# Performance work log

Hardware: AMD Instinct MI355X
Metric: run time of the kernel (lower is better)

The kernel has to match this reference:

```python
import jax, jax.numpy as jnp
import numpy as np

NZ, N_GEN = 128, 10
H1, H2, IMG = 512, 1024, 784
BATCH = 4096


def setup_inputs() -> dict:
    key = jax.random.key(0)
    ks = jax.random.split(key, 5)
    z = jax.random.normal(ks[0], (BATCH, NZ), dtype=jnp.float32)
    g_idx = jax.random.randint(ks[1], (BATCH,), 0, N_GEN)
    # stacked per-generator MLP weights (fan-in scaled init)
    W1 = jax.random.normal(ks[2], (N_GEN, NZ, H1), dtype=jnp.float32) / np.sqrt(NZ)
    b1 = jnp.zeros((N_GEN, H1), dtype=jnp.float32)
    W2 = jax.random.normal(ks[3], (N_GEN, H1, H2), dtype=jnp.float32) / np.sqrt(H1)
    b2 = jnp.zeros((N_GEN, H2), dtype=jnp.float32)
    W3 = jax.random.normal(ks[4], (N_GEN, H2, IMG), dtype=jnp.float32) / np.sqrt(H2)
    b3 = jnp.zeros((N_GEN, IMG), dtype=jnp.float32)
    return {"z": z, "g_idx": g_idx, "W1": W1, "b1": b1, "W2": W2, "b2": b2, "W3": W3, "b3": b3}


def reference(z, g_idx, W1, b1, W2, b2, W3, b3):
    # Run ALL n_gen sub-generators for every sample (as the torch module does),
    # then gather the chosen branch per sample.
    h = jax.nn.relu(jnp.einsum('bz,gzh->bgh', z, W1) + b1)          # [B, G, H1]
    h = jax.nn.relu(jnp.einsum('bgh,ghk->bgk', h, W2) + b2)         # [B, G, H2]
    images = jnp.tanh(jnp.einsum('bgk,gki->bgi', h, W3) + b3)       # [B, G, IMG]
    # images[arange(B), g_idx]
    out = jnp.take_along_axis(images, g_idx[:, None, None], axis=1)[:, 0]  # [B, IMG]
    return out
```

## Files before the change

### kernel.cpp

```cpp
#include <hip/hip_runtime.h>
#include <math.h>

#define NZ    128
#define H1    512
#define H2    1024
#define IMG   784
#define IMGP  896
#define BATCH 4096
#define NGEN  10
#define MPAD  128

typedef _Float16 f16;
typedef __attribute__((ext_vector_type(8))) _Float16 half8;
typedef __attribute__((ext_vector_type(4))) float floatx4;

#define TB1 ((NZ / 64) * (H1 / 64) * NGEN)
#define TB2 ((H1 / 64) * (H2 / 64) * NGEN)
#define TB3 ((H2 / 64) * (IMGP / 64) * NGEN)

__device__ __forceinline__ void cp16(void* l, const void* g) {
    __builtin_amdgcn_global_load_lds((const __attribute__((address_space(1))) void*)g,
                                     (__attribute__((address_space(3))) void*)l, 16, 0, 0);
}

template<int K, int N, int NPAD>
__device__ __forceinline__ void t_tile(int idx, const float* __restrict__ W,
                                       f16* __restrict__ Wt, f16 (*L)[72]) {
    constexpr int KT = K / 64, NT = NPAD / 64;
    const int g  = idx / (KT * NT);
    const int r2 = idx % (KT * NT);
    const int k0 = (r2 % KT) * 64;
    const int n0 = (r2 / KT) * 64;
    const int t = threadIdx.x;
    {
        const int kk0 = t >> 4;
        const int nq  = (t & 15) * 4;
        #pragma unroll
        for (int it = 0; it < 4; ++it) {
            const int kk = kk0 + it * 16;
            float4 v = make_float4(0.f, 0.f, 0.f, 0.f);
            if (n0 + nq < N)
                v = *(const float4*)(W + ((size_t)g * K + (k0 + kk)) * N + n0 + nq);
            L[nq + 0][kk] = (f16)v.x;
            L[nq + 1][kk] = (f16)v.y;
            L[nq + 2][kk] = (f16)v.z;
            L[nq + 3][kk] = (f16)v.w;
        }
    }
    __syncthreads();
    {
        const int nn0 = t >> 3;
        const int kq  = (t & 7) * 8;
        #pragma unroll
        for (int it = 0; it < 2; ++it) {
            const int nn = nn0 + it * 32;
            *(half8*)(Wt + ((size_t)g * NPAD + (n0 + nn)) * K + k0 + kq) =
                *(const half8*)&L[nn][kq];
        }
    }
}

__global__ __launch_bounds__(256)
void prep(const float* __restrict__ W1, const float* __restrict__ W2,
          const float* __restrict__ W3, f16* __restrict__ W1t,
          f16* __restrict__ W2t, f16* __restrict__ W3t,
          const int* __restrict__ g_idx, int* __restrict__ seg,
          int* __restrict__ perm) {
    __shared__ f16 L[64][72];
    __shared__ int lc[NGEN];
    __shared__ int lb[NGEN + 1];
    int bid = blockIdx.x;
    if (bid == 0) {
        const int t = threadIdx.x;
        if (t < NGEN) lc[t] = 0;
        __syncthreads();
        int gv[BATCH / 256];
        #pragma unroll
        for (int i = 0; i < BATCH / 256; ++i) {
            gv[i] = g_idx[t + i * 256];
            atomicAdd(&lc[gv[i]], 1);
        }
        __syncthreads();
        if (t == 0) {
            int s = 0;
            for (int g = 0; g < NGEN; ++g) { lb[g] = s; s += lc[g]; }
            lb[NGEN] = s;
        }
        __syncthreads();
        if (t <= NGEN) seg[t] = lb[t];
        if (t < NGEN) lc[t] = lb[t];
        __syncthreads();
        #pragma unroll
        for (int i = 0; i < BATCH / 256; ++i) {
            int p = atomicAdd(&lc[gv[i]], 1);
            perm[p] = t + i * 256;
        }
        return;
    }
    --bid;
    if (bid < TB1) { t_tile<NZ, H1, H1>(bid, W1, W1t, L); return; }
    bid -= TB1;
    if (bid < TB2) { t_tile<H1, H2, H2>(bid, W2, W2t, L); return; }
    bid -= TB2;
    t_tile<H2, IMG, IMGP>(bid, W3, W3t, L);
}

template<int K, int NOUT, int NPADB, int NM, int NN, int ACT, int SCATTER>
__global__ __launch_bounds__(256)
void gemm128(const f16* __restrict__ Ap, const f16* __restrict__ Wt,
             const float* __restrict__ bias, f16* __restrict__ Ch,
             float* __restrict__ Cout, const int* __restrict__ seg,
             const int* __restrict__ perm) {
    constexpr int NT  = K / 64;
    constexpr int NWG = NM * NN * NGEN;
    static_assert(NWG % 8 == 0, "gen-chunk swizzle needs NWG % 8 == 0");
    static_assert(NT >= 2, "pipeline assumes K >= 128");
    constexpr int CHUNK = NWG / 8;

    const int H = blockIdx.x;
    const int L = (H & 7) * CHUNK + (H >> 3);
    const int g   = L / (NM * NN);
    const int rem = L - g * (NM * NN);
    const int nt  = rem / NM;
    const int mt0 = rem - nt * NM;
    const int s0 = seg[g];
    const int ng = seg[g + 1] - s0;
    const int m0 = mt0 * 128;
    if (m0 >= ng) return;
    const int n0 = nt * 128;

    __shared__ f16 As[2 * 128 * 64];
    __shared__ f16 Bs[2 * 128 * 64];

    const int tid = threadIdx.x, lane = tid & 63, w = tid >> 6;

    const f16* ga[4]; const f16* gb[4]; int lo[4];
    #pragma unroll
    for (int j = 0; j < 4; ++j) {
        const int r   = w * 32 + j * 8 + (lane >> 3);
        const int swz = ((lane & 7) ^ ((r >> 1) & 7)) * 8;
        ga[j] = Ap + (size_t)(s0 + m0 + r) * K + swz;
        gb[j] = Wt + ((size_t)g * NPADB + n0 + r) * K + swz;
        lo[j] = (w * 32 + j * 8) * 64;
    }

    const int wm = (w & 1) * 64, wn = (w >> 1) * 64;
    const int lm = lane & 15, lq = lane >> 4;

    const int c = n0 + wn + 2 * lm;
    const bool in0 = (!SCATTER) || (c < NOUT);
    const bool in1 = (!SCATTER) || (c + 32 < NOUT);
    const float* bg = bias + (size_t)g * NOUT;
    const float bv0 = in0 ? bg[c]      : 0.f;
    const float bv1 = in0 ? bg[c + 1]  : 0.f;
    const float bv2 = in1 ? bg[c + 32] : 0.f;
    const float bv3 = in1 ? bg[c + 33] : 0.f;

    floatx4 acc[4][4] = {};

    auto stage = [&](int t, int b) {
        #pragma unroll
        for (int j = 0; j < 4; ++j) cp16(&As[b * 8192 + lo[j]], ga[j] + (size_t)t * 64);
        #pragma unroll
        for (int j = 0; j < 4; ++j) cp16(&Bs[b * 8192 + lo[j]], gb[j] + (size_t)t * 64);
    };
    stage(0, 0);
    __builtin_amdgcn_sched_barrier(0);
    stage(1, 1);

    for (int kc = 0; kc < NT; ++kc) {
        if (kc + 1 < NT) asm volatile("s_waitcnt vmcnt(8)" ::: "memory");
        else             asm volatile("s_waitcnt vmcnt(0)" ::: "memory");
        __builtin_amdgcn_sched_barrier(0);
        __builtin_amdgcn_s_barrier();
        __builtin_amdgcn_sched_barrier(0);

        const int cb = (kc & 1) * 8192;
        half8 a[2][4], b[2][4];
        #pragma unroll
        for (int ks = 0; ks < 2; ++ks) {
            #pragma unroll
            for (int mt = 0; mt < 4; ++mt) {
                const int r  = wm + mt * 16 + lm;
                const int pq = (ks * 4 + lq) ^ ((r >> 1) & 7);
                a[ks][mt] = *(const half8*)&As[cb + r * 64 + pq * 8];
            }
            #pragma unroll
            for (int nf = 0; nf < 4; ++nf) {
                const int r  = wn + (nf >> 1) * 32 + 2 * lm + (nf & 1);
                const int pq = (ks * 4 + lq) ^ ((r >> 1) & 7);
                b[ks][nf] = *(const half8*)&Bs[cb + r * 64 + pq * 8];
            }
        }
        asm volatile("s_waitcnt lgkmcnt(0)" ::: "memory");
        __builtin_amdgcn_sched_barrier(0);
        if (kc + 2 < NT) {
            __builtin_amdgcn_s_barrier();
            __builtin_amdgcn_sched_barrier(0);
            stage(kc + 2, kc & 1);
        }
        #pragma unroll
        for (int ks = 0; ks < 2; ++ks)
            #pragma unroll
            for (int mt = 0; mt < 4; ++mt)
                #pragma unroll
                for (int nf = 0; nf < 4; ++nf)
                    acc[mt][nf] = __builtin_amdgcn_mfma_f32_16x16x32_f16(
                        a[ks][mt], b[ks][nf], acc[mt][nf], 0, 0, 0);
    }

    #pragma unroll
    for (int mt = 0; mt < 4; ++mt)
        #pragma unroll
        for (int rr = 0; rr < 4; ++rr) {
            const int gr = m0 + wm + mt * 16 + lq * 4 + rr;
            if (gr >= ng) continue;
            float x0 = acc[mt][0][rr] + bv0;
            float x1 = acc[mt][1][rr] + bv1;
            float x2 = acc[mt][2][rr] + bv2;
            float x3 = acc[mt][3][rr] + bv3;
            if (ACT == 0) {
                x0 = fmaxf(x0, 0.f); x1 = fmaxf(x1, 0.f);
                x2 = fmaxf(x2, 0.f); x3 = fmaxf(x3, 0.f);
            } else {
                const float e0 = __expf(2.f * x0);
                const float e1 = __expf(2.f * x1);
                const float e2 = __expf(2.f * x2);
                const float e3 = __expf(2.f * x3);
                x0 = 1.f - 2.f / (e0 + 1.f);
                x1 = 1.f - 2.f / (e1 + 1.f);
                x2 = 1.f - 2.f / (e2 + 1.f);
                x3 = 1.f - 2.f / (e3 + 1.f);
            }
            if (SCATTER) {
                const size_t orow = (size_t)perm[s0 + gr];
                if (in0) *(float2*)&Cout[orow * NOUT + c]      = make_float2(x0, x1);
                if (in1) *(float2*)&Cout[orow * NOUT + c + 32] = make_float2(x2, x3);
            } else {
                union { uint u; f16 h[2]; } o0, o1;
                o0.h[0] = (f16)x0; o0.h[1] = (f16)x1;
                o1.h[0] = (f16)x2; o1.h[1] = (f16)x3;
                *(uint*)&Ch[(size_t)(s0 + gr) * NOUT + c]      = o0.u;
                *(uint*)&Ch[(size_t)(s0 + gr) * NOUT + c + 32] = o1.u;
            }
        }
}

__global__ __launch_bounds__(256)
void gemm_l1(const float* __restrict__ Az, const f16* __restrict__ Wt,
             const float* __restrict__ bias, f16* __restrict__ Ch,
             const int* __restrict__ seg, const int* __restrict__ perm) {
    constexpr int K = NZ, NOUT = H1, NPADB = H1, NM = 8, NN = 4;
    constexpr int NWG = NM * NN * NGEN, CHUNK = NWG / 8;
    const int H = blockIdx.x;
    const int L = (H & 7) * CHUNK + (H >> 3);
    const int g   = L / (NM * NN);
    const int rem = L - g * (NM * NN);
    const int nt  = rem / NM;
    const int mt0 = rem - nt * NM;
    const int s0 = seg[g];
    const int ng = seg[g + 1] - s0;
    const int m0 = mt0 * 128;
    if (m0 >= ng) return;
    const int n0 = nt * 128;

    __shared__ f16 As[2 * 8192];
    __shared__ f16 Bs[2 * 8192];
    const int tid = threadIdx.x, lane = tid & 63, w = tid >> 6;

    #pragma unroll
    for (int j = 0; j < 4; ++j) {
        const int r   = w * 32 + j * 8 + (lane >> 3);
        const int swz = ((lane & 7) ^ ((r >> 1) & 7)) * 8;
        const f16* gbj = Wt + ((size_t)g * NPADB + n0 + r) * K + swz;
        const int  loj = (w * 32 + j * 8) * 64;
        cp16(&Bs[loj],        gbj);
        cp16(&Bs[8192 + loj], gbj + 64);
    }
    int prow[4];
    #pragma unroll
    for (int p = 0; p < 4; ++p) {
        const int r = w * 32 + p * 8 + (lane >> 3);
        prow[p] = perm[min(s0 + m0 + r, BATCH - 1)];
    }
    #pragma unroll
    for (int t = 0; t < 2; ++t)
        #pragma unroll
        for (int p = 0; p < 4; ++p) {
            const int r = w * 32 + p * 8 + (lane >> 3);
            const float* src = Az + (size_t)prow[p] * K + t * 64 + (lane & 7) * 8;
            const float4 v0 = *(const float4*)src;
            const float4 v1 = *(const float4*)(src + 4);
            half8 h;
            h[0] = (f16)v0.x; h[1] = (f16)v0.y; h[2] = (f16)v0.z; h[3] = (f16)v0.w;
            h[4] = (f16)v1.x; h[5] = (f16)v1.y; h[6] = (f16)v1.z; h[7] = (f16)v1.w;
            const int pq = (lane & 7) ^ ((r >> 1) & 7);
            *(half8*)&As[t * 8192 + r * 64 + pq * 8] = h;
        }

    const int wm = (w & 1) * 64, wn = (w >> 1) * 64;
    const int lm = lane & 15, lq = lane >> 4;
    const int c = n0 + wn + 2 * lm;
    const float* bg = bias + (size_t)g * NOUT;
    const float bv0 = bg[c], bv1 = bg[c + 1], bv2 = bg[c + 32], bv3 = bg[c + 33];

    __syncthreads();

    floatx4 acc[4][4] = {};
    #pragma unroll
    for (int kc = 0; kc < 2; ++kc) {
        const int cb = kc * 8192;
        half8 a[2][4], b[2][4];
        #pragma unroll
        for (int ks = 0; ks < 2; ++ks) {
            #pragma unroll
            for (int mt = 0; mt < 4; ++mt) {
                const int r  = wm + mt * 16 + lm;
                const int pq = (ks * 4 + lq) ^ ((r >> 1) & 7);
                a[ks][mt] = *(const half8*)&As[cb + r * 64 + pq * 8];
            }
            #pragma unroll
            for (int nf = 0; nf < 4; ++nf) {
                const int r  = wn + (nf >> 1) * 32 + 2 * lm + (nf & 1);
                const int pq = (ks * 4 + lq) ^ ((r >> 1) & 7);
                b[ks][nf] = *(const half8*)&Bs[cb + r * 64 + pq * 8];
            }
        }
        #pragma unroll
        for (int ks = 0; ks < 2; ++ks)
            #pragma unroll
            for (int mt = 0; mt < 4; ++mt)
                #pragma unroll
                for (int nf = 0; nf < 4; ++nf)
                    acc[mt][nf] = __builtin_amdgcn_mfma_f32_16x16x32_f16(
                        a[ks][mt], b[ks][nf], acc[mt][nf], 0, 0, 0);
    }

    #pragma unroll
    for (int mt = 0; mt < 4; ++mt)
        #pragma unroll
        for (int rr = 0; rr < 4; ++rr) {
            const int gr = m0 + wm + mt * 16 + lq * 4 + rr;
            if (gr >= ng) continue;
            float x0 = fmaxf(acc[mt][0][rr] + bv0, 0.f);
            float x1 = fmaxf(acc[mt][1][rr] + bv1, 0.f);
            float x2 = fmaxf(acc[mt][2][rr] + bv2, 0.f);
            float x3 = fmaxf(acc[mt][3][rr] + bv3, 0.f);
            union { uint u; f16 h[2]; } o0, o1;
            o0.h[0] = (f16)x0; o0.h[1] = (f16)x1;
            o1.h[0] = (f16)x2; o1.h[1] = (f16)x3;
            *(uint*)&Ch[(size_t)(s0 + gr) * NOUT + c]      = o0.u;
            *(uint*)&Ch[(size_t)(s0 + gr) * NOUT + c + 32] = o1.u;
        }
}

extern "C" void kernel_launch(void* const* d_in, const int* in_sizes, int n_in,
                              void* d_out, int out_size, void* d_ws, size_t ws_size,
                              hipStream_t stream) {
    const float* z    = (const float*)d_in[0];
    const int*   gidx = (const int*)  d_in[1];
    const float* W1   = (const float*)d_in[2];
    const float* b1   = (const float*)d_in[3];
    const float* W2   = (const float*)d_in[4];
    const float* b2   = (const float*)d_in[5];
    const float* W3   = (const float*)d_in[6];
    const float* b3   = (const float*)d_in[7];
    float* out = (float*)d_out;

    char* ws = (char*)d_ws;
    size_t off = 0;
    auto alloc = [&](size_t bytes) { size_t o = off; off = (off + bytes + 255) & ~255ULL; return o; };
    int* seg  = (int*)(ws + alloc((size_t)(NGEN + 1) * 4));
    int* perm = (int*)(ws + alloc((size_t)(BATCH + MPAD) * 4));
    f16* h1p = (f16*)(ws + alloc((size_t)(BATCH + MPAD) * H1 * 2));
    f16* h2p = (f16*)(ws + alloc((size_t)(BATCH + MPAD) * H2 * 2));
    f16* W1t = (f16*)(ws + alloc((size_t)NGEN * H1 * NZ * 2));
    f16* W2t = (f16*)(ws + alloc((size_t)NGEN * H2 * H1 * 2));
    f16* W3t = (f16*)(ws + alloc((size_t)NGEN * IMGP * H2 * 2));

    prep<<<dim3(1 + TB1 + TB2 + TB3), dim3(256), 0, stream>>>(
        W1, W2, W3, W1t, W2t, W3t, gidx, seg, perm);

    gemm_l1<<<dim3(8 * 4 * NGEN), dim3(256), 0, stream>>>(
        z, W1t, b1, h1p, seg, perm);
    gemm128<H1, H2, H2, 8, 8, 0, 0><<<dim3(8 * 8 * NGEN), dim3(256), 0, stream>>>(
        h1p, W2t, b2, h2p, nullptr, seg, perm);
    gemm128<H2, IMG, IMGP, 8, 7, 1, 1><<<dim3(8 * 7 * NGEN), dim3(256), 0, stream>>>(
        h2p, W3t, b3, nullptr, out, seg, perm);
}
```

Measured before the change: 155.4 us.

## Fuse prep and three GEMM layers into one persistent kernel with grid barriers

Replaces the four separate launches with a single persistent kernel of 512 workgroups that moves through phases separated by atomic grid barriers. Each weight transpose is overlapped with the previous layer's GEMM. GEMM tiles are enumerated only for live row blocks per generator, so no workgroups launch just to exit. This removes launch gaps and idle tail time but adds barrier spin cost and a memset. It also relies on all 512 workgroups being co-resident (two per CU) to avoid deadlock.

```diff
diff --git a/kernel.cpp b/kernel.cpp
--- a/kernel.cpp
+++ b/kernel.cpp
@@ -9,6 +9,7 @@
 #define BATCH 4096
 #define NGEN  10
 #define MPAD  128
+#define NWORK 512
 
 typedef _Float16 f16;
 typedef __attribute__((ext_vector_type(8))) _Float16 half8;
@@ -23,9 +24,25 @@
                                      (__attribute__((address_space(3))) void*)l, 16, 0, 0);
 }
 
+__device__ __forceinline__ void gridbar(int* bar, int phase) {
+    __syncthreads();
+    if (threadIdx.x == 0) {
+        __threadfence();
+        __hip_atomic_fetch_add(&bar[phase], 1, __ATOMIC_RELEASE,
+                               __HIP_MEMORY_SCOPE_AGENT);
+        while (__hip_atomic_load(&bar[phase], __ATOMIC_ACQUIRE,
+                                 __HIP_MEMORY_SCOPE_AGENT) < NWORK)
+            __builtin_amdgcn_s_sleep(8);
+        __threadfence();
+    }
+    __syncthreads();
+}
+
 template<int K, int N, int NPAD>
-__device__ __forceinline__ void t_tile(int idx, const float* __restrict__ W,
-                                       f16* __restrict__ Wt, f16 (*L)[72]) {
+__device__ void t_item(int idx, const float* __restrict__ W,
+                       f16* __restrict__ Wt, char* smraw) {
+    f16 (*L)[72] = (f16(*)[72])smraw;
+    __syncthreads();
     constexpr int KT = K / 64, NT = NPAD / 64;
     const int g  = idx / (KT * NT);
     const int r2 = idx % (KT * NT);
@@ -60,79 +77,78 @@
     }
 }
 
-__global__ __launch_bounds__(256)
-void prep(const float* __restrict__ W1, const float* __restrict__ W2,
-          const float* __restrict__ W3, f16* __restrict__ W1t,
-          f16* __restrict__ W2t, f16* __restrict__ W3t,
-          const int* __restrict__ g_idx, int* __restrict__ seg,
-          int* __restrict__ perm) {
-    __shared__ f16 L[64][72];
-    __shared__ int lc[NGEN];
-    __shared__ int lb[NGEN + 1];
-    int bid = blockIdx.x;
-    if (bid == 0) {
-        const int t = threadIdx.x;
-        if (t < NGEN) lc[t] = 0;
-        __syncthreads();
-        int gv[BATCH / 256];
-        #pragma unroll
-        for (int i = 0; i < BATCH / 256; ++i) {
-            gv[i] = g_idx[t + i * 256];
-            atomicAdd(&lc[gv[i]], 1);
-        }
-        __syncthreads();
-        if (t == 0) {
-            int s = 0;
-            for (int g = 0; g < NGEN; ++g) { lb[g] = s; s += lc[g]; }
-            lb[NGEN] = s;
-        }
-        __syncthreads();
-        if (t <= NGEN) seg[t] = lb[t];
-        if (t < NGEN) lc[t] = lb[t];
-        __syncthreads();
-        #pragma unroll
-        for (int i = 0; i < BATCH / 256; ++i) {
-            int p = atomicAdd(&lc[gv[i]], 1);
-            perm[p] = t + i * 256;
-        }
-        return;
-    }
-    --bid;
-    if (bid < TB1) { t_tile<NZ, H1, H1>(bid, W1, W1t, L); return; }
-    bid -= TB1;
-    if (bid < TB2) { t_tile<H1, H2, H2>(bid, W2, W2t, L); return; }
-    bid -= TB2;
-    t_tile<H2, IMG, IMGP>(bid, W3, W3t, L);
-}
-
-template<int K, int NOUT, int NPADB, int NM, int NN, int ACT, int SCATTER>
-__global__ __launch_bounds__(256)
-void gemm128(const f16* __restrict__ Ap, const f16* __restrict__ Wt,
-             const float* __restrict__ bias, f16* __restrict__ Ch,
-             float* __restrict__ Cout, const int* __restrict__ seg,
-             const int* __restrict__ perm) {
-    constexpr int NT  = K / 64;
-    constexpr int NWG = NM * NN * NGEN;
-    static_assert(NWG % 8 == 0, "gen-chunk swizzle needs NWG % 8 == 0");
-    static_assert(NT >= 2, "pipeline assumes K >= 128");
-    constexpr int CHUNK = NWG / 8;
-
-    const int H = blockIdx.x;
-    const int L = (H & 7) * CHUNK + (H >> 3);
-    const int g   = L / (NM * NN);
-    const int rem = L - g * (NM * NN);
-    const int nt  = rem / NM;
-    const int mt0 = rem - nt * NM;
-    const int s0 = seg[g];
-    const int ng = seg[g + 1] - s0;
-    const int m0 = mt0 * 128;
-    if (m0 >= ng) return;
-    const int n0 = nt * 128;
-
-    __shared__ f16 As[2 * 128 * 64];
-    __shared__ f16 Bs[2 * 128 * 64];
-
+__device__ void hist_item(const int* __restrict__ g_idx, int* __restrict__ seg,
+                          int* __restrict__ perm, char* smraw) {
+    int* lc = (int*)smraw;
+    int* lb = lc + NGEN;
+    const int t = threadIdx.x;
+    __syncthreads();
+    if (t < NGEN) lc[t] = 0;
+    __syncthreads();
+    int gv[BATCH / 256];
+    #pragma unroll
+    for (int i = 0; i < BATCH / 256; ++i) {
+        gv[i] = g_idx[t + i * 256];
+        atomicAdd(&lc[gv[i]], 1);
+    }
+    __syncthreads();
+    if (t == 0) {
+        int s = 0;
+        #pragma unroll
+        for (int g = 0; g < NGEN; ++g) { lb[g] = s; s += lc[g]; }
+        lb[NGEN] = s;
+    }
+    __syncthreads();
+    if (t <= NGEN) seg[t] = lb[t];
+    if (t < NGEN) lc[t] = lb[t];
+    __syncthreads();
+    #pragma unroll
+    for (int i = 0; i < BATCH / 256; ++i) {
+        int p = atomicAdd(&lc[gv[i]], 1);
+        perm[p] = t + i * 256;
+    }
+}
+
+template<int NN>
+__device__ __forceinline__ int live_total(const int* __restrict__ seg) {
+    int s = 0;
+    #pragma unroll
+    for (int g = 0; g < NGEN; ++g)
+        s += (((seg[g + 1] - seg[g]) + 127) >> 7) * NN;
+    return s;
+}
+template<int NN>
+__device__ __forceinline__ void item_to_tile(const int* __restrict__ seg, int i,
+                                             int& g, int& s0, int& ng,
+                                             int& m0, int& n0) {
+    int base = 0;
+    #pragma unroll
+    for (int gg = 0; gg < NGEN; ++gg) {
+        const int s = seg[gg], e = seg[gg + 1];
+        const int cm = ((e - s) + 127) >> 7;
+        const int c  = cm * NN;
+        if (i >= base && i < base + c) {
+            const int loc = i - base;
+            g = gg; s0 = s; ng = e - s;
+            m0 = (loc % cm) * 128;
+            n0 = (loc / cm) * 128;
+        }
+        base += c;
+    }
+}
+
+template<int K, int NOUT, int NPADB, int ACT, int SCATTER>
+__device__ void gemm_item(int g, int s0, int ng, int m0, int n0,
+                          const f16* __restrict__ Ap, const f16* __restrict__ Wt,
+                          const float* __restrict__ bias, f16* __restrict__ Ch,
+                          float* __restrict__ Cout, const int* __restrict__ perm,
+                          char* smraw) {
+    constexpr int NT = K / 64;
+    f16* As = (f16*)smraw;
+    f16* Bs = (f16*)(smraw + 32768);
     const int tid = threadIdx.x, lane = tid & 63, w = tid >> 6;
+
+    __syncthreads();
 
     const f16* ga[4]; const f16* gb[4]; int lo[4];
     #pragma unroll
@@ -143,7 +159,6 @@
         gb[j] = Wt + ((size_t)g * NPADB + n0 + r) * K + swz;
         lo[j] = (w * 32 + j * 8) * 64;
     }
-
     const int wm = (w & 1) * 64, wn = (w >> 1) * 64;
     const int lm = lane & 15, lq = lane >> 4;
 
@@ -246,27 +261,16 @@
         }
 }
 
-__global__ __launch_bounds__(256)
-void gemm_l1(const float* __restrict__ Az, const f16* __restrict__ Wt,
-             const float* __restrict__ bias, f16* __restrict__ Ch,
-             const int* __restrict__ seg, const int* __restrict__ perm) {
-    constexpr int K = NZ, NOUT = H1, NPADB = H1, NM = 8, NN = 4;
-    constexpr int NWG = NM * NN * NGEN, CHUNK = NWG / 8;
-    const int H = blockIdx.x;
-    const int L = (H & 7) * CHUNK + (H >> 3);
-    const int g   = L / (NM * NN);
-    const int rem = L - g * (NM * NN);
-    const int nt  = rem / NM;
-    const int mt0 = rem - nt * NM;
-    const int s0 = seg[g];
-    const int ng = seg[g + 1] - s0;
-    const int m0 = mt0 * 128;
-    if (m0 >= ng) return;
-    const int n0 = nt * 128;
-
-    __shared__ f16 As[2 * 8192];
-    __shared__ f16 Bs[2 * 8192];
+__device__ void l1_item(int g, int s0, int ng, int m0, int n0,
+                        const float* __restrict__ Az, const f16* __restrict__ Wt,
+                        const float* __restrict__ bias, f16* __restrict__ Ch,
+                        const int* __restrict__ perm, char* smraw) {
+    constexpr int K = NZ, NOUT = H1, NPADB = H1;
+    f16* As = (f16*)smraw;
+    f16* Bs = (f16*)(smraw + 32768);
     const int tid = threadIdx.x, lane = tid & 63, w = tid >> 6;
+
+    __syncthreads();
 
     #pragma unroll
     for (int j = 0; j < 4; ++j) {
@@ -354,6 +358,58 @@
         }
 }
 
+__global__ __launch_bounds__(256, 2)
+void fused(const float* __restrict__ z, const int* __restrict__ gidx,
+           const float* __restrict__ W1, const float* __restrict__ b1,
+           const float* __restrict__ W2, const float* __restrict__ b2,
+           const float* __restrict__ W3, const float* __restrict__ b3,
+           float* __restrict__ out, int* seg, int* perm,
+           f16* h1p, f16* h2p, f16* W1t, f16* W2t, f16* W3t, int* bar) {
+    __shared__ __align__(16) char sm[65536];
+    const int bid = blockIdx.x;
+
+    for (int i = bid; i < 1 + TB1; i += NWORK) {
+        if (i == 0) hist_item(gidx, seg, perm, sm);
+        else        t_item<NZ, H1, H1>(i - 1, W1, W1t, sm);
+    }
+    gridbar(bar, 0);
+
+    {
+        const int nl = live_total<H1 / 128>(seg);
+        for (int i = bid; i < nl + TB2; i += NWORK) {
+            if (i < nl) {
+                int g, s0, ng, m0, n0;
+                item_to_tile<H1 / 128>(seg, i, g, s0, ng, m0, n0);
+                l1_item(g, s0, ng, m0, n0, z, W1t, b1, h1p, perm, sm);
+            } else t_item<H1, H2, H2>(i - nl, W2, W2t, sm);
+        }
+    }
+    gridbar(bar, 1);
+
+    {
+        const int nl = live_total<H2 / 128>(seg);
+        for (int i = bid; i < nl + TB3; i += NWORK) {
+            if (i < nl) {
+                int g, s0, ng, m0, n0;
+                item_to_tile<H2 / 128>(seg, i, g, s0, ng, m0, n0);
+                gemm_item<H1, H2, H2, 0, 0>(g, s0, ng, m0, n0, h1p, W2t, b2,
+                                            h2p, nullptr, perm, sm);
+            } else t_item<H2, IMG, IMGP>(i - nl, W3, W3t, sm);
+        }
+    }
+    gridbar(bar, 2);
+
+    {
+        const int nl = live_total<IMGP / 128>(seg);
+        for (int i = bid; i < nl; i += NWORK) {
+            int g, s0, ng, m0, n0;
+            item_to_tile<IMGP / 128>(seg, i, g, s0, ng, m0, n0);
+            gemm_item<H2, IMG, IMGP, 1, 1>(g, s0, ng, m0, n0, h2p, W3t, b3,
+                                           nullptr, out, perm, sm);
+        }
+    }
+}
+
 extern "C" void kernel_launch(void* const* d_in, const int* in_sizes, int n_in,
                               void* d_out, int out_size, void* d_ws, size_t ws_size,
                               hipStream_t stream) {
@@ -377,14 +433,11 @@
     f16* W1t = (f16*)(ws + alloc((size_t)NGEN * H1 * NZ * 2));
     f16* W2t = (f16*)(ws + alloc((size_t)NGEN * H2 * H1 * 2));
     f16* W3t = (f16*)(ws + alloc((size_t)NGEN * IMGP * H2 * 2));
-
-    prep<<<dim3(1 + TB1 + TB2 + TB3), dim3(256), 0, stream>>>(
-        W1, W2, W3, W1t, W2t, W3t, gidx, seg, perm);
-
-    gemm_l1<<<dim3(8 * 4 * NGEN), dim3(256), 0, stream>>>(
-        z, W1t, b1, h1p, seg, perm);
-    gemm128<H1, H2, H2, 8, 8, 0, 0><<<dim3(8 * 8 * NGEN), dim3(256), 0, stream>>>(
-        h1p, W2t, b2, h2p, nullptr, seg, perm);
-    gemm128<H2, IMG, IMGP, 8, 7, 1, 1><<<dim3(8 * 7 * NGEN), dim3(256), 0, stream>>>(
-        h2p, W3t, b3, nullptr, out, seg, perm);
-}
+    int* bar = (int*)(ws + alloc(256));
+
+    hipMemsetAsync(bar, 0, 256, stream);
+
+    fused<<<dim3(NWORK), dim3(256), 0, stream>>>(
+        z, gidx, W1, b1, W2, b2, W3, b3, out,
+        seg, perm, h1p, h2p, W1t, W2t, W3t, bar);
+}
```

After: 435.1 us. 180% more time.

## Switch grouped GEMM to K=32 tiles with a four-stage LDS ring

Applied to the files above, without the earlier changes.

The grouped GEMM for layers 2 and 3 now steps through K in chunks of 32 instead of 64. It keeps four LDS buffers and prefetches three stages ahead, which lets it drop the second barrier per iteration and issue the next stage right after the first barrier. The swizzle and B-row mapping are reworked for the 32-wide rows. This deepens the copy pipeline and reduces barrier stalls, but it doubles the number of loop iterations and barriers per tile, with fewer MFMAs between syncs.

```diff
diff --git a/kernel.cpp b/kernel.cpp
--- a/kernel.cpp
+++ b/kernel.cpp
@@ -107,20 +107,20 @@
 
 template<int K, int NOUT, int NPADB, int NM, int NN, int ACT, int SCATTER>
 __global__ __launch_bounds__(256)
-void gemm128(const f16* __restrict__ Ap, const f16* __restrict__ Wt,
-             const float* __restrict__ bias, f16* __restrict__ Ch,
-             float* __restrict__ Cout, const int* __restrict__ seg,
-             const int* __restrict__ perm) {
-    constexpr int NT  = K / 64;
+void gemm32(const f16* __restrict__ Ap, const f16* __restrict__ Wt,
+            const float* __restrict__ bias, f16* __restrict__ Ch,
+            float* __restrict__ Cout, const int* __restrict__ seg,
+            const int* __restrict__ perm) {
+    constexpr int NT  = K / 32;
+    static_assert(NT >= 4, "pipeline assumes K >= 128");
     constexpr int NWG = NM * NN * NGEN;
     static_assert(NWG % 8 == 0, "gen-chunk swizzle needs NWG % 8 == 0");
-    static_assert(NT >= 2, "pipeline assumes K >= 128");
     constexpr int CHUNK = NWG / 8;
 
-    const int H = blockIdx.x;
-    const int L = (H & 7) * CHUNK + (H >> 3);
-    const int g   = L / (NM * NN);
-    const int rem = L - g * (NM * NN);
+    const int Hh = blockIdx.x;
+    const int Lw = (Hh & 7) * CHUNK + (Hh >> 3);
+    const int g   = Lw / (NM * NN);
+    const int rem = Lw - g * (NM * NN);
     const int nt  = rem / NM;
     const int mt0 = rem - nt * NM;
     const int s0 = seg[g];
@@ -129,19 +129,20 @@
     if (m0 >= ng) return;
     const int n0 = nt * 128;
 
-    __shared__ f16 As[2 * 128 * 64];
-    __shared__ f16 Bs[2 * 128 * 64];
+    __shared__ f16 As[4 * 4096];
+    __shared__ f16 Bs[4 * 4096];
 
     const int tid = threadIdx.x, lane = tid & 63, w = tid >> 6;
 
-    const f16* ga[4]; const f16* gb[4]; int lo[4];
-    #pragma unroll
-    for (int j = 0; j < 4; ++j) {
-        const int r   = w * 32 + j * 8 + (lane >> 3);
-        const int swz = ((lane & 7) ^ ((r >> 1) & 7)) * 8;
-        ga[j] = Ap + (size_t)(s0 + m0 + r) * K + swz;
-        gb[j] = Wt + ((size_t)g * NPADB + n0 + r) * K + swz;
-        lo[j] = (w * 32 + j * 8) * 64;
+    const f16* ga[2]; const f16* gb[2]; int lo[2];
+    #pragma unroll
+    for (int j = 0; j < 2; ++j) {
+        const int l = w * 32 + j * 16 + (lane >> 2);
+        const int q = (lane & 3) ^ ((l >> 1) & 3);
+        ga[j] = Ap + (size_t)(s0 + m0 + l) * K + q * 8;
+        const int tb = w * 32 + 2 * (lane >> 2) + j;
+        gb[j] = Wt + ((size_t)g * NPADB + n0 + tb) * K + q * 8;
+        lo[j] = (w * 32 + j * 16) * 32;
     }
 
     const int wm = (w & 1) * 64, wn = (w >> 1) * 64;
@@ -158,55 +159,50 @@
 
     floatx4 acc[4][4] = {};
 
-    auto stage = [&](int t, int b) {
-        #pragma unroll
-        for (int j = 0; j < 4; ++j) cp16(&As[b * 8192 + lo[j]], ga[j] + (size_t)t * 64);
-        #pragma unroll
-        for (int j = 0; j < 4; ++j) cp16(&Bs[b * 8192 + lo[j]], gb[j] + (size_t)t * 64);
+    auto stage = [&](int b) {
+        #pragma unroll
+        for (int j = 0; j < 2; ++j) { cp16(&As[b * 4096 + lo[j]], ga[j]); ga[j] += 32; }
+        #pragma unroll
+        for (int j = 0; j < 2; ++j) { cp16(&Bs[b * 4096 + lo[j]], gb[j]); gb[j] += 32; }
     };
-    stage(0, 0);
+    stage(0);
     __builtin_amdgcn_sched_barrier(0);
-    stage(1, 1);
+    stage(1);
+    __builtin_amdgcn_sched_barrier(0);
+    stage(2);
 
     for (int kc = 0; kc < NT; ++kc) {
-        if (kc + 1 < NT) asm volatile("s_waitcnt vmcnt(8)" ::: "memory");
-        else             asm volatile("s_waitcnt vmcnt(0)" ::: "memory");
+        const int left = NT - 1 - kc;
+        if (left >= 2)      asm volatile("s_waitcnt vmcnt(8)" ::: "memory");
+        else if (left == 1) asm volatile("s_waitcnt vmcnt(4)" ::: "memory");
+        else                asm volatile("s_waitcnt vmcnt(0)" ::: "memory");
         __builtin_amdgcn_sched_barrier(0);
         __builtin_amdgcn_s_barrier();
         __builtin_amdgcn_sched_barrier(0);
-
-        const int cb = (kc & 1) * 8192;
-        half8 a[2][4], b[2][4];
-        #pragma unroll
-        for (int ks = 0; ks < 2; ++ks) {
-            #pragma unroll
-            for (int mt = 0; mt < 4; ++mt) {
-                const int r  = wm + mt * 16 + lm;
-                const int pq = (ks * 4 + lq) ^ ((r >> 1) & 7);
-                a[ks][mt] = *(const half8*)&As[cb + r * 64 + pq * 8];
-            }
-            #pragma unroll
-            for (int nf = 0; nf < 4; ++nf) {
-                const int r  = wn + (nf >> 1) * 32 + 2 * lm + (nf & 1);
-                const int pq = (ks * 4 + lq) ^ ((r >> 1) & 7);
-                b[ks][nf] = *(const half8*)&Bs[cb + r * 64 + pq * 8];
-            }
+        if (kc + 3 < NT) stage((kc + 3) & 3);
+
+        const int cb = (kc & 3) * 4096;
+        half8 a[4], b[4];
+        #pragma unroll
+        for (int mt = 0; mt < 4; ++mt) {
+            const int r  = wm + mt * 16 + lm;
+            const int pq = lq ^ ((r >> 1) & 3);
+            a[mt] = *(const half8*)&As[cb + r * 32 + pq * 8];
+        }
+        #pragma unroll
+        for (int nf = 0; nf < 4; ++nf) {
+            const int l  = wn + (nf >> 1) * 32 + (nf & 1) * 16 + lm;
+            const int pq = lq ^ ((l >> 1) & 3);
+            b[nf] = *(const half8*)&Bs[cb + l * 32 + pq * 8];
         }
         asm volatile("s_waitcnt lgkmcnt(0)" ::: "memory");
         __builtin_amdgcn_sched_barrier(0);
-        if (kc + 2 < NT) {
-            __builtin_amdgcn_s_barrier();
-            __builtin_amdgcn_sched_barrier(0);
-            stage(kc + 2, kc & 1);
-        }
-        #pragma unroll
-        for (int ks = 0; ks < 2; ++ks)
+        #pragma unroll
+        for (int mt = 0; mt < 4; ++mt)
             #pragma unroll
-            for (int mt = 0; mt < 4; ++mt)
-                #pragma unroll
-                for (int nf = 0; nf < 4; ++nf)
-                    acc[mt][nf] = __builtin_amdgcn_mfma_f32_16x16x32_f16(
-                        a[ks][mt], b[ks][nf], acc[mt][nf], 0, 0, 0);
+            for (int nf = 0; nf < 4; ++nf)
+                acc[mt][nf] = __builtin_amdgcn_mfma_f32_16x16x32_f16(
+                    a[mt], b[nf], acc[mt][nf], 0, 0, 0);
     }
 
     #pragma unroll
@@ -252,10 +248,10 @@
              const int* __restrict__ seg, const int* __restrict__ perm) {
     constexpr int K = NZ, NOUT = H1, NPADB = H1, NM = 8, NN = 4;
     constexpr int NWG = NM * NN * NGEN, CHUNK = NWG / 8;
-    const int H = blockIdx.x;
-    const int L = (H & 7) * CHUNK + (H >> 3);
-    const int g   = L / (NM * NN);
-    const int rem = L - g * (NM * NN);
+    const int Hh = blockIdx.x;
+    const int Lw = (Hh & 7) * CHUNK + (Hh >> 3);
+    const int g   = Lw / (NM * NN);
+    const int rem = Lw - g * (NM * NN);
     const int nt  = rem / NM;
     const int mt0 = rem - nt * NM;
     const int s0 = seg[g];
@@ -383,8 +379,8 @@
 
     gemm_l1<<<dim3(8 * 4 * NGEN), dim3(256), 0, stream>>>(
         z, W1t, b1, h1p, seg, perm);
-    gemm128<H1, H2, H2, 8, 8, 0, 0><<<dim3(8 * 8 * NGEN), dim3(256), 0, stream>>>(
+    gemm32<H1, H2, H2, 8, 8, 0, 0><<<dim3(8 * 8 * NGEN), dim3(256), 0, stream>>>(
         h1p, W2t, b2, h2p, nullptr, seg, perm);
-    gemm128<H2, IMG, IMGP, 8, 7, 1, 1><<<dim3(8 * 7 * NGEN), dim3(256), 0, stream>>>(
+    gemm32<H2, IMG, IMGP, 8, 7, 1, 1><<<dim3(8 * 7 * NGEN), dim3(256), 0, stream>>>(
         h2p, W3t, b3, nullptr, out, seg, perm);
 }
```

Result: slower. 165.1 us (+6.3%).

## Overlap weight transposes with preceding GEMM layers and use 512-thread blocks

Applied to the files above, without the earlier changes.

The single prep kernel, which transposed all three weight stacks before any GEMM began, is split up. W2 conversion now runs inside the layer-1 launch and W3 conversion inside the layer-2 launch, so weight conversion overlaps the previous layer's matrix work. All GEMMs move to 512-thread blocks with 8 waves, each covering a 64x32 sub-tile, which halves the per-thread accumulator and fragment registers. The trade-offs are more waves sharing each tile's LDS traffic and a larger shared buffer per block. Layer 1 still reads W1t, which is produced by a separate preceding small kernel.

```diff
diff --git a/kernel.cpp b/kernel.cpp
--- a/kernel.cpp
+++ b/kernel.cpp
@@ -18,23 +18,26 @@
 #define TB2 ((H1 / 64) * (H2 / 64) * NGEN)
 #define TB3 ((H2 / 64) * (IMGP / 64) * NGEN)
 
+#define NWG1 (8 * 4 * NGEN)
+#define NWG2 (8 * 8 * NGEN)
+#define NWG3 (8 * 7 * NGEN)
+
 __device__ __forceinline__ void cp16(void* l, const void* g) {
     __builtin_amdgcn_global_load_lds((const __attribute__((address_space(1))) void*)g,
                                      (__attribute__((address_space(3))) void*)l, 16, 0, 0);
 }
 
 template<int K, int N, int NPAD>
-__device__ __forceinline__ void t_tile(int idx, const float* __restrict__ W,
-                                       f16* __restrict__ Wt, f16 (*L)[72]) {
-    constexpr int KT = K / 64, NT = NPAD / 64;
-    const int g  = idx / (KT * NT);
-    const int r2 = idx % (KT * NT);
+__device__ void t_tile256(int idx, const float* __restrict__ W,
+                          f16* __restrict__ Wt, f16 (*L)[72]) {
+    constexpr int KT = K / 64, NTt = NPAD / 64;
+    const int g  = idx / (KT * NTt);
+    const int r2 = idx % (KT * NTt);
     const int k0 = (r2 % KT) * 64;
     const int n0 = (r2 / KT) * 64;
     const int t = threadIdx.x;
     {
-        const int kk0 = t >> 4;
-        const int nq  = (t & 15) * 4;
+        const int kk0 = t >> 4, nq = (t & 15) * 4;
         #pragma unroll
         for (int it = 0; it < 4; ++it) {
             const int kk = kk0 + it * 16;
@@ -49,8 +52,7 @@
     }
     __syncthreads();
     {
-        const int nn0 = t >> 3;
-        const int kq  = (t & 7) * 8;
+        const int nn0 = t >> 3, kq = (t & 7) * 8;
         #pragma unroll
         for (int it = 0; it < 2; ++it) {
             const int nn = nn0 + it * 32;
@@ -60,16 +62,47 @@
     }
 }
 
+template<int K, int N, int NPAD>
+__device__ void t_tile512(int idx, const float* __restrict__ W,
+                          f16* __restrict__ Wt, char* smraw) {
+    f16 (*L)[72] = (f16(*)[72])smraw;
+    constexpr int KT = K / 64, NTt = NPAD / 64;
+    const int g  = idx / (KT * NTt);
+    const int r2 = idx % (KT * NTt);
+    const int k0 = (r2 % KT) * 64;
+    const int n0 = (r2 / KT) * 64;
+    const int t = threadIdx.x;
+    {
+        const int kk0 = t >> 4;
+        const int nq  = (t & 15) * 4;
+        #pragma unroll
+        for (int it = 0; it < 2; ++it) {
+            const int kk = kk0 + it * 32;
+            float4 v = make_float4(0.f, 0.f, 0.f, 0.f);
+            if (n0 + nq < N)
+                v = *(const float4*)(W + ((size_t)g * K + (k0 + kk)) * N + n0 + nq);
+            L[nq + 0][kk] = (f16)v.x;
+            L[nq + 1][kk] = (f16)v.y;
+            L[nq + 2][kk] = (f16)v.z;
+            L[nq + 3][kk] = (f16)v.w;
+        }
+    }
+    __syncthreads();
+    {
+        const int nn = t >> 3, kq = (t & 7) * 8;
+        *(half8*)(Wt + ((size_t)g * NPAD + (n0 + nn)) * K + k0 + kq) =
+            *(const half8*)&L[nn][kq];
+    }
+}
+
 __global__ __launch_bounds__(256)
-void prep(const float* __restrict__ W1, const float* __restrict__ W2,
-          const float* __restrict__ W3, f16* __restrict__ W1t,
-          f16* __restrict__ W2t, f16* __restrict__ W3t,
-          const int* __restrict__ g_idx, int* __restrict__ seg,
-          int* __restrict__ perm) {
+void prep1(const float* __restrict__ W1, f16* __restrict__ W1t,
+           const int* __restrict__ g_idx, int* __restrict__ seg,
+           int* __restrict__ perm) {
     __shared__ f16 L[64][72];
     __shared__ int lc[NGEN];
     __shared__ int lb[NGEN + 1];
-    int bid = blockIdx.x;
+    const int bid = blockIdx.x;
     if (bid == 0) {
         const int t = threadIdx.x;
         if (t < NGEN) lc[t] = 0;
@@ -97,30 +130,18 @@
         }
         return;
     }
-    --bid;
-    if (bid < TB1) { t_tile<NZ, H1, H1>(bid, W1, W1t, L); return; }
-    bid -= TB1;
-    if (bid < TB2) { t_tile<H1, H2, H2>(bid, W2, W2t, L); return; }
-    bid -= TB2;
-    t_tile<H2, IMG, IMGP>(bid, W3, W3t, L);
+    t_tile256<NZ, H1, H1>(bid - 1, W1, W1t, L);
 }
 
 template<int K, int NOUT, int NPADB, int NM, int NN, int ACT, int SCATTER>
-__global__ __launch_bounds__(256)
-void gemm128(const f16* __restrict__ Ap, const f16* __restrict__ Wt,
-             const float* __restrict__ bias, f16* __restrict__ Ch,
-             float* __restrict__ Cout, const int* __restrict__ seg,
-             const int* __restrict__ perm) {
-    constexpr int NT  = K / 64;
-    constexpr int NWG = NM * NN * NGEN;
-    static_assert(NWG % 8 == 0, "gen-chunk swizzle needs NWG % 8 == 0");
-    static_assert(NT >= 2, "pipeline assumes K >= 128");
-    constexpr int CHUNK = NWG / 8;
-
-    const int H = blockIdx.x;
-    const int L = (H & 7) * CHUNK + (H >> 3);
-    const int g   = L / (NM * NN);
-    const int rem = L - g * (NM * NN);
+__device__ void gemm8(int Lw, const f16* __restrict__ Ap,
+                      const f16* __restrict__ Wt, const float* __restrict__ bias,
+                      f16* __restrict__ Ch, float* __restrict__ Cout,
+                      const int* __restrict__ seg, const int* __restrict__ perm,
+                      char* smraw) {
+    constexpr int NT = K / 64;
+    const int g   = Lw / (NM * NN);
+    const int rem = Lw - g * (NM * NN);
     const int nt  = rem / NM;
     const int mt0 = rem - nt * NM;
     const int s0 = seg[g];
@@ -129,54 +150,50 @@
     if (m0 >= ng) return;
     const int n0 = nt * 128;
 
-    __shared__ f16 As[2 * 128 * 64];
-    __shared__ f16 Bs[2 * 128 * 64];
-
+    f16* As = (f16*)smraw;
+    f16* Bs = (f16*)(smraw + 32768);
     const int tid = threadIdx.x, lane = tid & 63, w = tid >> 6;
 
-    const f16* ga[4]; const f16* gb[4]; int lo[4];
-    #pragma unroll
-    for (int j = 0; j < 4; ++j) {
-        const int r   = w * 32 + j * 8 + (lane >> 3);
+    const f16* ga[2]; const f16* gb[2]; int lo[2];
+    #pragma unroll
+    for (int j = 0; j < 2; ++j) {
+        const int r   = w * 16 + j * 8 + (lane >> 3);
         const int swz = ((lane & 7) ^ ((r >> 1) & 7)) * 8;
         ga[j] = Ap + (size_t)(s0 + m0 + r) * K + swz;
         gb[j] = Wt + ((size_t)g * NPADB + n0 + r) * K + swz;
-        lo[j] = (w * 32 + j * 8) * 64;
-    }
-
-    const int wm = (w & 1) * 64, wn = (w >> 1) * 64;
+        lo[j] = (w * 16 + j * 8) * 64;
+    }
+
+    const int wm = (w & 1) * 64, wn = (w >> 1) * 32;
     const int lm = lane & 15, lq = lane >> 4;
 
     const int c = n0 + wn + 2 * lm;
     const bool in0 = (!SCATTER) || (c < NOUT);
-    const bool in1 = (!SCATTER) || (c + 32 < NOUT);
     const float* bg = bias + (size_t)g * NOUT;
-    const float bv0 = in0 ? bg[c]      : 0.f;
-    const float bv1 = in0 ? bg[c + 1]  : 0.f;
-    const float bv2 = in1 ? bg[c + 32] : 0.f;
-    const float bv3 = in1 ? bg[c + 33] : 0.f;
-
-    floatx4 acc[4][4] = {};
+    const float bv0 = in0 ? bg[c]     : 0.f;
+    const float bv1 = in0 ? bg[c + 1] : 0.f;
+
+    floatx4 acc[4][2] = {};
 
     auto stage = [&](int t, int b) {
         #pragma unroll
-        for (int j = 0; j < 4; ++j) cp16(&As[b * 8192 + lo[j]], ga[j] + (size_t)t * 64);
-        #pragma unroll
-        for (int j = 0; j < 4; ++j) cp16(&Bs[b * 8192 + lo[j]], gb[j] + (size_t)t * 64);
+        for (int j = 0; j < 2; ++j) cp16(&As[b * 8192 + lo[j]], ga[j] + (size_t)t * 64);
+        #pragma unroll
+        for (int j = 0; j < 2; ++j) cp16(&Bs[b * 8192 + lo[j]], gb[j] + (size_t)t * 64);
     };
     stage(0, 0);
     __builtin_amdgcn_sched_barrier(0);
     stage(1, 1);
 
     for (int kc = 0; kc < NT; ++kc) {
-        if (kc + 1 < NT) asm volatile("s_waitcnt vmcnt(8)" ::: "memory");
+        if (kc + 1 < NT) asm volatile("s_waitcnt vmcnt(4)" ::: "memory");
         else             asm volatile("s_waitcnt vmcnt(0)" ::: "memory");
         __builtin_amdgcn_sched_barrier(0);
         __builtin_amdgcn_s_barrier();
         __builtin_amdgcn_sched_barrier(0);
 
         const int cb = (kc & 1) * 8192;
-        half8 a[2][4], b[2][4];
+        half8 a[2][4], b[2][2];
         #pragma unroll
         for (int ks = 0; ks < 2; ++ks) {
             #pragma unroll
@@ -186,8 +203,8 @@
                 a[ks][mt] = *(const half8*)&As[cb + r * 64 + pq * 8];
             }
             #pragma unroll
-            for (int nf = 0; nf < 4; ++nf) {
-                const int r  = wn + (nf >> 1) * 32 + 2 * lm + (nf & 1);
+            for (int nf = 0; nf < 2; ++nf) {
+                const int r  = wn + 2 * lm + nf;
                 const int pq = (ks * 4 + lq) ^ ((r >> 1) & 7);
                 b[ks][nf] = *(const half8*)&Bs[cb + r * 64 + pq * 8];
             }
@@ -204,7 +221,7 @@
             #pragma unroll
             for (int mt = 0; mt < 4; ++mt)
                 #pragma unroll
-                for (int nf = 0; nf < 4; ++nf)
+                for (int nf = 0; nf < 2; ++nf)
                     acc[mt][nf] = __builtin_amdgcn_mfma_f32_16x16x32_f16(
                         a[ks][mt], b[ks][nf], acc[mt][nf], 0, 0, 0);
     }
@@ -217,45 +234,34 @@
             if (gr >= ng) continue;
             float x0 = acc[mt][0][rr] + bv0;
             float x1 = acc[mt][1][rr] + bv1;
-            float x2 = acc[mt][2][rr] + bv2;
-            float x3 = acc[mt][3][rr] + bv3;
             if (ACT == 0) {
                 x0 = fmaxf(x0, 0.f); x1 = fmaxf(x1, 0.f);
-                x2 = fmaxf(x2, 0.f); x3 = fmaxf(x3, 0.f);
             } else {
                 const float e0 = __expf(2.f * x0);
                 const float e1 = __expf(2.f * x1);
-                const float e2 = __expf(2.f * x2);
-                const float e3 = __expf(2.f * x3);
                 x0 = 1.f - 2.f / (e0 + 1.f);
                 x1 = 1.f - 2.f / (e1 + 1.f);
-                x2 = 1.f - 2.f / (e2 + 1.f);
-                x3 = 1.f - 2.f / (e3 + 1.f);
             }
             if (SCATTER) {
-                const size_t orow = (size_t)perm[s0 + gr];
-                if (in0) *(float2*)&Cout[orow * NOUT + c]      = make_float2(x0, x1);
-                if (in1) *(float2*)&Cout[orow * NOUT + c + 32] = make_float2(x2, x3);
+                if (in0) {
+                    const size_t orow = (size_t)perm[s0 + gr];
+                    *(float2*)&Cout[orow * NOUT + c] = make_float2(x0, x1);
+                }
             } else {
-                union { uint u; f16 h[2]; } o0, o1;
-                o0.h[0] = (f16)x0; o0.h[1] = (f16)x1;
-                o1.h[0] = (f16)x2; o1.h[1] = (f16)x3;
-                *(uint*)&Ch[(size_t)(s0 + gr) * NOUT + c]      = o0.u;
-                *(uint*)&Ch[(size_t)(s0 + gr) * NOUT + c + 32] = o1.u;
-            }
-        }
-}
-
-__global__ __launch_bounds__(256)
-void gemm_l1(const float* __restrict__ Az, const f16* __restrict__ Wt,
-             const float* __restrict__ bias, f16* __restrict__ Ch,
-             const int* __restrict__ seg, const int* __restrict__ perm) {
+                union { uint u; f16 h[2]; } o;
+                o.h[0] = (f16)x0; o.h[1] = (f16)x1;
+                *(uint*)&Ch[(size_t)(s0 + gr) * NOUT + c] = o.u;
+            }
+        }
+}
+
+__device__ void l1_item(int Lw, const float* __restrict__ Az,
+                        const f16* __restrict__ Wt, const float* __restrict__ bias,
+                        f16* __restrict__ Ch, const int* __restrict__ seg,
+                        const int* __restrict__ perm, char* smraw) {
     constexpr int K = NZ, NOUT = H1, NPADB = H1, NM = 8, NN = 4;
-    constexpr int NWG = NM * NN * NGEN, CHUNK = NWG / 8;
-    const int H = blockIdx.x;
-    const int L = (H & 7) * CHUNK + (H >> 3);
-    const int g   = L / (NM * NN);
-    const int rem = L - g * (NM * NN);
+    const int g   = Lw / (NM * NN);
+    const int rem = Lw - g * (NM * NN);
     const int nt  = rem / NM;
     const int mt0 = rem - nt * NM;
     const int s0 = seg[g];
@@ -264,53 +270,50 @@
     if (m0 >= ng) return;
     const int n0 = nt * 128;
 
-    __shared__ f16 As[2 * 8192];
-    __shared__ f16 Bs[2 * 8192];
+    f16* As = (f16*)smraw;
+    f16* Bs = (f16*)(smraw + 32768);
     const int tid = threadIdx.x, lane = tid & 63, w = tid >> 6;
 
     #pragma unroll
-    for (int j = 0; j < 4; ++j) {
-        const int r   = w * 32 + j * 8 + (lane >> 3);
+    for (int j = 0; j < 2; ++j) {
+        const int r   = w * 16 + j * 8 + (lane >> 3);
         const int swz = ((lane & 7) ^ ((r >> 1) & 7)) * 8;
         const f16* gbj = Wt + ((size_t)g * NPADB + n0 + r) * K + swz;
-        const int  loj = (w * 32 + j * 8) * 64;
+        const int  loj = (w * 16 + j * 8) * 64;
         cp16(&Bs[loj],        gbj);
         cp16(&Bs[8192 + loj], gbj + 64);
     }
-    int prow[4];
-    #pragma unroll
-    for (int p = 0; p < 4; ++p) {
-        const int r = w * 32 + p * 8 + (lane >> 3);
-        prow[p] = perm[min(s0 + m0 + r, BATCH - 1)];
-    }
-    #pragma unroll
-    for (int t = 0; t < 2; ++t)
-        #pragma unroll
-        for (int p = 0; p < 4; ++p) {
-            const int r = w * 32 + p * 8 + (lane >> 3);
-            const float* src = Az + (size_t)prow[p] * K + t * 64 + (lane & 7) * 8;
+    const int arow = tid >> 3, aq = tid & 7;
+    #pragma unroll
+    for (int p = 0; p < 2; ++p) {
+        const int r   = arow + p * 64;
+        const int prw = perm[min(s0 + m0 + r, BATCH - 1)];
+        #pragma unroll
+        for (int t = 0; t < 2; ++t) {
+            const float* src = Az + (size_t)prw * K + t * 64 + aq * 8;
             const float4 v0 = *(const float4*)src;
             const float4 v1 = *(const float4*)(src + 4);
             half8 h;
             h[0] = (f16)v0.x; h[1] = (f16)v0.y; h[2] = (f16)v0.z; h[3] = (f16)v0.w;
             h[4] = (f16)v1.x; h[5] = (f16)v1.y; h[6] = (f16)v1.z; h[7] = (f16)v1.w;
-            const int pq = (lane & 7) ^ ((r >> 1) & 7);
+            const int pq = aq ^ ((r >> 1) & 7);
             *(half8*)&As[t * 8192 + r * 64 + pq * 8] = h;
         }
-
-    const int wm = (w & 1) * 64, wn = (w >> 1) * 64;
+    }
+
+    const int wm = (w & 1) * 64, wn = (w >> 1) * 32;
     const int lm = lane & 15, lq = lane >> 4;
     const int c = n0 + wn + 2 * lm;
     const float* bg = bias + (size_t)g * NOUT;
-    const float bv0 = bg[c], bv1 = bg[c + 1], bv2 = bg[c + 32], bv3 = bg[c + 33];
+    const float bv0 = bg[c], bv1 = bg[c + 1];
 
     __syncthreads();
 
-    floatx4 acc[4][4] = {};
+    floatx4 acc[4][2] = {};
     #pragma unroll
     for (int kc = 0; kc < 2; ++kc) {
         const int cb = kc * 8192;
-        half8 a[2][4], b[2][4];
+        half8 a[2][4], b[2][2];
         #pragma unroll
         for (int ks = 0; ks < 2; ++ks) {
             #pragma unroll
@@ -320,8 +323,8 @@
                 a[ks][mt] = *(const half8*)&As[cb + r * 64 + pq * 8];
             }
             #pragma unroll
-            for (int nf = 0; nf < 4; ++nf) {
-                const int r  = wn + (nf >> 1) * 32 + 2 * lm + (nf & 1);
+            for (int nf = 0; nf < 2; ++nf) {
+                const int r  = wn + 2 * lm + nf;
                 const int pq = (ks * 4 + lq) ^ ((r >> 1) & 7);
                 b[ks][nf] = *(const half8*)&Bs[cb + r * 64 + pq * 8];
             }
@@ -331,7 +334,7 @@
             #pragma unroll
             for (int mt = 0; mt < 4; ++mt)
                 #pragma unroll
-                for (int nf = 0; nf < 4; ++nf)
+                for (int nf = 0; nf < 2; ++nf)
                     acc[mt][nf] = __builtin_amdgcn_mfma_f32_16x16x32_f16(
                         a[ks][mt], b[ks][nf], acc[mt][nf], 0, 0, 0);
     }
@@ -342,16 +345,54 @@
         for (int rr = 0; rr < 4; ++rr) {
             const int gr = m0 + wm + mt * 16 + lq * 4 + rr;
             if (gr >= ng) continue;
-            float x0 = fmaxf(acc[mt][0][rr] + bv0, 0.f);
-            float x1 = fmaxf(acc[mt][1][rr] + bv1, 0.f);
-            float x2 = fmaxf(acc[mt][2][rr] + bv2, 0.f);
-            float x3 = fmaxf(acc[mt][3][rr] + bv3, 0.f);
-            union { uint u; f16 h[2]; } o0, o1;
-            o0.h[0] = (f16)x0; o0.h[1] = (f16)x1;
-            o1.h[0] = (f16)x2; o1.h[1] = (f16)x3;
-            *(uint*)&Ch[(size_t)(s0 + gr) * NOUT + c]      = o0.u;
-            *(uint*)&Ch[(size_t)(s0 + gr) * NOUT + c + 32] = o1.u;
-        }
+            const float x0 = fmaxf(acc[mt][0][rr] + bv0, 0.f);
+            const float x1 = fmaxf(acc[mt][1][rr] + bv1, 0.f);
+            union { uint u; f16 h[2]; } o;
+            o.h[0] = (f16)x0; o.h[1] = (f16)x1;
+            *(uint*)&Ch[(size_t)(s0 + gr) * NOUT + c] = o.u;
+        }
+}
+
+__global__ __launch_bounds__(512)
+void l1f(const float* __restrict__ z, const f16* __restrict__ W1t,
+         const float* __restrict__ b1, f16* __restrict__ h1p,
+         const float* __restrict__ W2, f16* __restrict__ W2t,
+         const int* __restrict__ seg, const int* __restrict__ perm) {
+    __shared__ __align__(16) char sm[65536];
+    const int bid = blockIdx.x;
+    if (bid < NWG1) {
+        const int Lw = (bid & 7) * (NWG1 / 8) + (bid >> 3);
+        l1_item(Lw, z, W1t, b1, h1p, seg, perm, sm);
+    } else {
+        t_tile512<H1, H2, H2>(bid - NWG1, W2, W2t, sm);
+    }
+}
+
+__global__ __launch_bounds__(512)
+void g2f(const f16* __restrict__ h1p, const f16* __restrict__ W2t,
+         const float* __restrict__ b2, f16* __restrict__ h2p,
+         const float* __restrict__ W3, f16* __restrict__ W3t,
+         const int* __restrict__ seg, const int* __restrict__ perm) {
+    __shared__ __align__(16) char sm[65536];
+    const int bid = blockIdx.x;
+    if (bid < NWG2) {
+        const int Lw = (bid & 7) * (NWG2 / 8) + (bid >> 3);
+        gemm8<H1, H2, H2, 8, 8, 0, 0>(Lw, h1p, W2t, b2, h2p, nullptr,
+                                      seg, perm, sm);
+    } else {
+        t_tile512<H2, IMG, IMGP>(bid - NWG2, W3, W3t, sm);
+    }
+}
+
+__global__ __launch_bounds__(512)
+void g3k(const f16* __restrict__ h2p, const f16* __restrict__ W3t,
+         const float* __restrict__ b3, float* __restrict__ out,
+         const int* __restrict__ seg, const int* __restrict__ perm) {
+    __shared__ __align__(16) char sm[65536];
+    const int bid = blockIdx.x;
+    const int Lw = (bid & 7) * (NWG3 / 8) + (bid >> 3);
+    gemm8<H2, IMG, IMGP, 8, 7, 1, 1>(Lw, h2p, W3t, b3, nullptr, out,
+                                     seg, perm, sm);
 }
 
 extern "C" void kernel_launch(void* const* d_in, const int* in_sizes, int n_in,
@@ -378,13 +419,10 @@
     f16* W2t = (f16*)(ws + alloc((size_t)NGEN * H2 * H1 * 2));
     f16* W3t = (f16*)(ws + alloc((size_t)NGEN * IMGP * H2 * 2));
 
-    prep<<<dim3(1 + TB1 + TB2 + TB3), dim3(256), 0, stream>>>(
-        W1, W2, W3, W1t, W2t, W3t, gidx, seg, perm);
-
-    gemm_l1<<<dim3(8 * 4 * NGEN), dim3(256), 0, stream>>>(
-        z, W1t, b1, h1p, seg, perm);
-    gemm128<H1, H2, H2, 8, 8, 0, 0><<<dim3(8 * 8 * NGEN), dim3(256), 0, stream>>>(
-        h1p, W2t, b2, h2p, nullptr, seg, perm);
-    gemm128<H2, IMG, IMGP, 8, 7, 1, 1><<<dim3(8 * 7 * NGEN), dim3(256), 0, stream>>>(
-        h2p, W3t, b3, nullptr, out, seg, perm);
-}
+    prep1<<<dim3(1 + TB1), dim3(256), 0, stream>>>(W1, W1t, gidx, seg, perm);
+    l1f<<<dim3(NWG1 + TB2), dim3(512), 0, stream>>>(z, W1t, b1, h1p, W2, W2t,
+                                                    seg, perm);
+    g2f<<<dim3(NWG2 + TB3), dim3(512), 0, stream>>>(h1p, W2t, b2, h2p, W3, W3t,
+                                                    seg, perm);
+    g3k<<<dim3(NWG3), dim3(512), 0, stream>>>(h2p, W3t, b3, out, seg, perm);
+}
```

Measured after the change: 148.8 us. 4.3% less time.
